# Kernel optimization log

Measured on AMD Instinct MI355X. Metric: run time of the kernel, lower is better.

## Reference

```python
import jax, jax.numpy as jnp
import numpy as np

B, S, D = 2, 2048, 2048
H, DK, DV, L = 16, 128, 128, 64


def setup_inputs() -> dict:
    key = jax.random.key(0)
    ks = jax.random.split(key, 16)
    sc = lambda fan_in: 1.0 / np.sqrt(fan_in)
    inp = {
        "queries": jax.random.normal(ks[0], (B, S, D), jnp.float32),
        "keys": jax.random.normal(ks[1], (B, S, D), jnp.float32),
        "values": jax.random.normal(ks[2], (B, S, D), jnp.float32),
        # weights stored [in, out]
        "Wq": jax.random.normal(ks[3], (D, DK * H), jnp.float32) * sc(D),
        "bq": jnp.zeros((DK * H,), jnp.float32),
        "Wlk": jax.random.normal(ks[4], (D, L * H), jnp.float32) * sc(D),
        "blk": jnp.zeros((L * H,), jnp.float32),
        "Wlv": jax.random.normal(ks[5], (D, L * H), jnp.float32) * sc(D),
        "blv": jnp.zeros((L * H,), jnp.float32),
        "Wkr": jax.random.normal(ks[6], (L, DK), jnp.float32) * sc(L),
        "bkr": jnp.zeros((DK,), jnp.float32),
        "Wvr": jax.random.normal(ks[7], (L, DV), jnp.float32) * sc(L),
        "bvr": jnp.zeros((DV,), jnp.float32),
        "Wo": jax.random.normal(ks[8], (DV * H, D), jnp.float32) * sc(DV * H),
        "bo": jnp.zeros((D,), jnp.float32),
    }
    return inp


def reference(queries, keys, values, Wq, bq, Wlk, blk, Wlv, blv, Wkr, bkr, Wvr, bvr, Wo, bo):
    b, sq, _ = queries.shape
    sk = keys.shape[1]
    # query projection -> [b, h, sq, dk]
    q = (queries @ Wq + bq).reshape(b, sq, H, DK).transpose(0, 2, 1, 3)
    # low-rank latent KV -> [b, sk, h, L]
    lat_k = (keys @ Wlk + blk).reshape(b, sk, H, L)
    lat_v = (values @ Wlv + blv).reshape(b, sk, H, L)
    # reconstruction -> [b, h, sk, dk/dv]
    k = (lat_k @ Wkr + bkr).transpose(0, 2, 1, 3)
    v = (lat_v @ Wvr + bvr).transpose(0, 2, 1, 3)
    scores = jnp.einsum("bhqd,bhkd->bhqk", q, k) / np.sqrt(DK).astype(np.float32)
    causal = jnp.triu(jnp.ones((sq, sk), dtype=bool), k=1)
    scores = jnp.where(causal, -jnp.inf, scores)
    attn = jax.nn.softmax(scores, axis=-1)
    out = jnp.einsum("bhqk,bhkd->bhqd", attn, v)
    out = out.transpose(0, 2, 1, 3).reshape(b, sq, H * DV)
    return out @ Wo + bo
```

## Files before the change

kernel.cpp:

```cpp
#include <hip/hip_runtime.h>
#include <hip/hip_bf16.h>

#define B_SZ    2
#define S_LEN   2048
#define D_MODEL 2048
#define N_HEADS 16
#define D_HEAD  128
#define L_RANK  64
#define M_ROWS  (B_SZ * S_LEN)
#define KD      2048
#define NT      (KD / 32)

typedef short          bf16x8 __attribute__((ext_vector_type(8)));
typedef float          f32x4  __attribute__((ext_vector_type(4)));
typedef float          f32x16 __attribute__((ext_vector_type(16)));
typedef unsigned short us4v   __attribute__((ext_vector_type(4)));
typedef unsigned short us8v   __attribute__((ext_vector_type(8)));
typedef unsigned int   u32x4  __attribute__((ext_vector_type(4)));

#define SCALE_Q 0.127517432f

static __device__ __forceinline__ unsigned short f2bf(float f) {
    unsigned int u = __float_as_uint(f);
    u += 0x7FFFu + ((u >> 16) & 1u);
    return (unsigned short)(u >> 16);
}

static __device__ __forceinline__ void gload16(const void* g, void* l) {
    __builtin_amdgcn_global_load_lds(
        (const __attribute__((address_space(1))) unsigned int*)g,
        (__attribute__((address_space(3))) unsigned int*)l, 16, 0, 0);
}

static __device__ __forceinline__ float exp2_hw(float x) {
    float r; asm("v_exp_f32 %0, %1" : "=v"(r) : "v"(x)); return r;
}
static __device__ __forceinline__ unsigned int cvtpk_bf16(float a, float b) {
    unsigned int r; asm("v_cvt_pk_bf16_f32 %0, %1, %2" : "=v"(r) : "v"(a), "v"(b)); return r;
}

__global__ __launch_bounds__(256) void prep_kernel(
    const float* __restrict__ q_in, const float* __restrict__ k_in,
    const float* __restrict__ v_in,
    const float* __restrict__ Wq, const float* __restrict__ Wlk,
    const float* __restrict__ Wlv, const float* __restrict__ Wo,
    const float* __restrict__ Wkr, const float* __restrict__ Wvr,
    unsigned short* __restrict__ q_o, unsigned short* __restrict__ k_o,
    unsigned short* __restrict__ v_o,
    unsigned short* __restrict__ WqT, unsigned short* __restrict__ WlkT,
    unsigned short* __restrict__ WlvT, unsigned short* __restrict__ WoT,
    unsigned short* __restrict__ WkrT, unsigned short* __restrict__ WvrT)
{
    __shared__ float tl[64][69];
    const int bid = blockIdx.x, tid = threadIdx.x;

    if (bid < 12288) {
        const int z = bid >> 12;
        const float* in = z == 0 ? q_in : (z == 1 ? k_in : v_in);
        unsigned short* out = z == 0 ? q_o : (z == 1 ? k_o : v_o);
        size_t i = ((size_t)(bid & 4095) * 256 + tid) * 8;
        float4 a = *(const float4*)&in[i];
        float4 b = *(const float4*)&in[i + 4];
        us8v o = { f2bf(a.x), f2bf(a.y), f2bf(a.z), f2bf(a.w),
                   f2bf(b.x), f2bf(b.y), f2bf(b.z), f2bf(b.w) };
        *(us8v*)&out[i] = o;
    } else if (bid < 16384) {
        const int t = bid - 12288;
        const int z = t >> 10;
        const int y = (t & 1023) >> 5, x = t & 31;
        const int Nz = (z == 1 || z == 2) ? 1024 : 2048;
        if (x * 64 >= Nz) return;
        const float* W = z == 0 ? Wq : (z == 1 ? Wlk : (z == 2 ? Wlv : Wo));
        unsigned short* WT = z == 0 ? WqT : (z == 1 ? WlkT : (z == 2 ? WlvT : WoT));
        const int k0 = y * 64, n0 = x * 64;
        #pragma unroll
        for (int c = 0; c < 4; ++c) {
            int idx = c * 256 + tid;
            int r = idx >> 4, c4 = (idx & 15) * 4;
            float4 v = *(const float4*)&W[(size_t)(k0 + r) * Nz + n0 + c4];
            tl[r][c4] = v.x; tl[r][c4 + 1] = v.y; tl[r][c4 + 2] = v.z; tl[r][c4 + 3] = v.w;
        }
        __syncthreads();
        #pragma unroll
        for (int c = 0; c < 2; ++c) {
            int idx = c * 256 + tid;
            int nr = idx >> 3, s = idx & 7;
            us8v o;
            #pragma unroll
            for (int j = 0; j < 8; ++j) o[j] = f2bf(tl[s * 8 + j][nr]);
            *(us8v*)&WT[(size_t)(n0 + nr) * KD + k0 + s * 8] = o;
        }
    } else {
        #pragma unroll 1
        for (int t2 = 0; t2 < 2; ++t2) {
            const float* W = t2 ? Wvr : Wkr;
            unsigned short* WT = t2 ? WvrT : WkrT;
            for (int i = 0; i < 32; ++i) {
                int e = i * 256 + tid;
                int d = e >> 6, l = e & 63;
                WT[d * 64 + l] = f2bf(W[l * 128 + d]);
            }
        }
    }
}

__global__ __launch_bounds__(256) void stage1_kernel(
    const unsigned short* __restrict__ Aq, const unsigned short* __restrict__ Ak,
    const unsigned short* __restrict__ Av,
    const unsigned short* __restrict__ WqT, const unsigned short* __restrict__ WlkT,
    const unsigned short* __restrict__ WlvT,
    const float* __restrict__ bq, const float* __restrict__ blk,
    const float* __restrict__ blv,
    unsigned short* __restrict__ q_bf, unsigned short* __restrict__ lat_k,
    unsigned short* __restrict__ lat_v)
{
    __shared__ unsigned short Al[2][128 * 32];
    __shared__ unsigned short Bl[2][128 * 32];

    const int flat = blockIdx.x;
    const int swz = (flat & 7) * 128 + (flat >> 3);
    int z, rem;
    if (swz < 512)      { z = 0; rem = swz; }
    else if (swz < 768) { z = 1; rem = swz - 512; }
    else                { z = 2; rem = swz - 768; }
    int row0, col0, Nz;
    if (z == 0) { row0 = (rem >> 4) * 128; col0 = (rem & 15) * 128; Nz = 2048; }
    else        { row0 = (rem >> 3) * 128; col0 = (rem & 7) * 128;  Nz = 1024; }

    const unsigned short* A    = z == 0 ? Aq  : (z == 1 ? Ak   : Av);
    const unsigned short* Bt   = z == 0 ? WqT : (z == 1 ? WlkT : WlvT);
    const float*          bias = z == 0 ? bq  : (z == 1 ? blk  : blv);
    unsigned short*       C    = z == 0 ? q_bf : (z == 1 ? lat_k : lat_v);

    const int tid = threadIdx.x;
    const int lane = tid & 63, wid = tid >> 6;
    const int lr = lane & 15, lg = lane >> 4;
    const int wr = wid >> 1, wc = wid & 1;

    const unsigned short* ag[2];
    const unsigned short* bg[2];
    unsigned short* alp[2][2];
    unsigned short* blp[2][2];
    #pragma unroll
    for (int c = 0; c < 2; ++c) {
        int idx = wid * 128 + c * 64 + lane;
        int row = idx >> 2, p = idx & 3;
        int sp = p ^ ((row >> 1) & 3);
        ag[c] = A  + (size_t)(row0 + row) * KD + sp * 8;
        bg[c] = Bt + (size_t)(col0 + row) * KD + sp * 8;
        alp[0][c] = Al[0] + idx * 8;  alp[1][c] = Al[1] + idx * 8;
        blp[0][c] = Bl[0] + idx * 8;  blp[1][c] = Bl[1] + idx * 8;
    }
    const int sx = (lr >> 1) & 3;
    const int abase = (wr * 64 + lr) * 32 + ((lg ^ sx) * 8);
    const int bbase = (wc * 64 + lr) * 32 + ((lg ^ sx) * 8);

    f32x4 acc[4][4];
    #pragma unroll
    for (int m = 0; m < 4; ++m)
        #pragma unroll
        for (int n = 0; n < 4; ++n) acc[m][n] = (f32x4){0.f, 0.f, 0.f, 0.f};

    #pragma unroll
    for (int c = 0; c < 2; ++c) { gload16(ag[c], alp[0][c]); gload16(bg[c], blp[0][c]); }
    __syncthreads();

    #pragma unroll 1
    for (int t = 0; t < NT; ++t) {
        const int cur = t & 1, nxt = cur ^ 1;
        if (t + 1 < NT) {
            #pragma unroll
            for (int c = 0; c < 2; ++c) {
                gload16(ag[c] + (size_t)(t + 1) * 32, alp[nxt][c]);
                gload16(bg[c] + (size_t)(t + 1) * 32, blp[nxt][c]);
            }
        }
        bf16x8 af[4], bfv[4];
        #pragma unroll
        for (int m = 0; m < 4; ++m) af[m]  = *(const bf16x8*)&Al[cur][abase + m * 512];
        #pragma unroll
        for (int n = 0; n < 4; ++n) bfv[n] = *(const bf16x8*)&Bl[cur][bbase + n * 512];
        __builtin_amdgcn_s_setprio(1);
        #pragma unroll
        for (int m = 0; m < 4; ++m)
            #pragma unroll
            for (int n = 0; n < 4; ++n)
                acc[m][n] = __builtin_amdgcn_mfma_f32_16x16x32_bf16(af[m], bfv[n], acc[m][n], 0, 0, 0);
        __builtin_amdgcn_s_setprio(0);
        __syncthreads();
    }

    float bv[4];
    #pragma unroll
    for (int n = 0; n < 4; ++n) bv[n] = bias[col0 + wc * 64 + n * 16 + lr];
    const float omul = (z == 0) ? SCALE_Q : 1.0f;

    #pragma unroll
    for (int m = 0; m < 4; ++m) {
        #pragma unroll
        for (int n = 0; n < 4; ++n) {
            const int col = col0 + wc * 64 + n * 16 + lr;
            const int rowb = row0 + wr * 64 + m * 16 + lg * 4;
            #pragma unroll
            for (int j = 0; j < 4; ++j)
                C[(size_t)(rowb + j) * Nz + col] = f2bf((acc[m][n][j] + bv[n]) * omul);
        }
    }
}

__global__ __launch_bounds__(256) void recon_kernel(
    const unsigned short* __restrict__ lat_k, const unsigned short* __restrict__ lat_v,
    const unsigned short* __restrict__ WkrT, const unsigned short* __restrict__ WvrT,
    const float* __restrict__ bkr, const float* __restrict__ bvr,
    unsigned short* __restrict__ k_bf, unsigned short* __restrict__ v_t)
{
    __shared__ unsigned short Alds[128 * 64];
    __shared__ unsigned short Blds[128 * 64];

    const int flat = blockIdx.x;
    const int swz = (flat & 7) * 128 + (flat >> 3);
    const int z = swz >> 9;
    const int rem = swz & 511;
    const int h = rem >> 5;
    const int r0 = (rem & 31) * 128;

    const unsigned short* lat = z ? lat_v : lat_k;
    const unsigned short* WT  = z ? WvrT : WkrT;
    const float* bias = z ? bvr : bkr;

    const int tid = threadIdx.x;
    const int lane = tid & 63, wid = tid >> 6;
    const int lr = lane & 15, lg = lane >> 4;
    const int wm = wid >> 1, wn = wid & 1;

    #pragma unroll
    for (int c = 0; c < 4; ++c) {
        int e = c * 256 + tid;
        int row = e >> 3, pc = e & 7;
        gload16(lat + (size_t)(r0 + row) * 1024 + h * 64 + ((pc ^ (row & 7)) * 8),
                Alds + e * 8);
    }
    #pragma unroll
    for (int c = 0; c < 4; ++c) {
        int e = c * 256 + tid;
        int d = e >> 3, pc = e & 7;
        gload16(WT + (size_t)d * 64 + ((pc ^ (d & 7)) * 8), Blds + e * 8);
    }
    __syncthreads();

    f32x4 acc[4][4];
    #pragma unroll
    for (int m = 0; m < 4; ++m)
        #pragma unroll
        for (int n = 0; n < 4; ++n) acc[m][n] = (f32x4){0.f, 0.f, 0.f, 0.f};

    #pragma unroll
    for (int ks = 0; ks < 2; ++ks) {
        bf16x8 af[4], bfv[4];
        #pragma unroll
        for (int m = 0; m < 4; ++m) {
            int row = wm * 64 + m * 16 + lr;
            af[m] = *(const bf16x8*)&Alds[row * 64 + (((ks * 4 + lg) ^ (row & 7)) * 8)];
        }
        #pragma unroll
        for (int n = 0; n < 4; ++n) {
            int row = wn * 64 + n * 16 + lr;
            bfv[n] = *(const bf16x8*)&Blds[row * 64 + (((ks * 4 + lg) ^ (row & 7)) * 8)];
        }
        #pragma unroll
        for (int m = 0; m < 4; ++m)
            #pragma unroll
            for (int n = 0; n < 4; ++n)
                acc[m][n] = __builtin_amdgcn_mfma_f32_16x16x32_bf16(af[m], bfv[n], acc[m][n], 0, 0, 0);
    }

    const int b = r0 >> 11;
    float bv[4];
    #pragma unroll
    for (int n = 0; n < 4; ++n) bv[n] = bias[wn * 64 + n * 16 + lr];

    #pragma unroll
    for (int m = 0; m < 4; ++m) {
        #pragma unroll
        for (int n = 0; n < 4; ++n) {
            const int d = wn * 64 + n * 16 + lr;
            const int rowb = r0 + wm * 64 + m * 16 + lg * 4;
            if (z == 0) {
                #pragma unroll
                for (int j = 0; j < 4; ++j)
                    k_bf[(size_t)(rowb + j) * D_MODEL + h * D_HEAD + d] =
                        f2bf(acc[m][n][j] + bv[n]);
            } else {
                us4v o = { f2bf(acc[m][n][0] + bv[n]), f2bf(acc[m][n][1] + bv[n]),
                           f2bf(acc[m][n][2] + bv[n]), f2bf(acc[m][n][3] + bv[n]) };
                *(us4v*)&v_t[((size_t)(b * 16 + h) * 128 + d) * 2048 + (rowb & 2047)] = o;
            }
        }
    }
}

__global__ __launch_bounds__(256) void out_gemm_kernel(
    const unsigned short* __restrict__ A,
    const unsigned short* __restrict__ Bt,
    const float* __restrict__ bias,
    float* __restrict__ C)
{
    __shared__ unsigned short Al[2][128 * 32];
    __shared__ unsigned short Bl[2][128 * 32];

    const int flat = blockIdx.x;
    const int swz = (flat & 7) * 64 + (flat >> 3);
    const int row0 = (swz >> 4) * 128, col0 = (swz & 15) * 128;

    const int tid = threadIdx.x;
    const int lane = tid & 63, wid = tid >> 6;
    const int lr = lane & 15, lg = lane >> 4;
    const int wr = wid >> 1, wc = wid & 1;

    const unsigned short* ag[2];
    const unsigned short* bg[2];
    unsigned short* alp[2][2];
    unsigned short* blp[2][2];
    #pragma unroll
    for (int c = 0; c < 2; ++c) {
        int idx = wid * 128 + c * 64 + lane;
        int row = idx >> 2, p = idx & 3;
        int sp = p ^ ((row >> 1) & 3);
        ag[c] = A  + (size_t)(row0 + row) * KD + sp * 8;
        bg[c] = Bt + (size_t)(col0 + row) * KD + sp * 8;
        alp[0][c] = Al[0] + idx * 8;  alp[1][c] = Al[1] + idx * 8;
        blp[0][c] = Bl[0] + idx * 8;  blp[1][c] = Bl[1] + idx * 8;
    }
    const int sx = (lr >> 1) & 3;
    const int abase = (wr * 64 + lr) * 32 + ((lg ^ sx) * 8);
    const int bbase = (wc * 64 + lr) * 32 + ((lg ^ sx) * 8);

    f32x4 acc[4][4];
    #pragma unroll
    for (int m = 0; m < 4; ++m)
        #pragma unroll
        for (int n = 0; n < 4; ++n) acc[m][n] = (f32x4){0.f, 0.f, 0.f, 0.f};

    #pragma unroll
    for (int c = 0; c < 2; ++c) { gload16(ag[c], alp[0][c]); gload16(bg[c], blp[0][c]); }
    __syncthreads();

    #pragma unroll 1
    for (int t = 0; t < NT; ++t) {
        const int cur = t & 1, nxt = cur ^ 1;
        if (t + 1 < NT) {
            #pragma unroll
            for (int c = 0; c < 2; ++c) {
                gload16(ag[c] + (size_t)(t + 1) * 32, alp[nxt][c]);
                gload16(bg[c] + (size_t)(t + 1) * 32, blp[nxt][c]);
            }
        }
        bf16x8 af[4], bfv[4];
        #pragma unroll
        for (int m = 0; m < 4; ++m) af[m]  = *(const bf16x8*)&Al[cur][abase + m * 512];
        #pragma unroll
        for (int n = 0; n < 4; ++n) bfv[n] = *(const bf16x8*)&Bl[cur][bbase + n * 512];
        __builtin_amdgcn_s_setprio(1);
        #pragma unroll
        for (int m = 0; m < 4; ++m)
            #pragma unroll
            for (int n = 0; n < 4; ++n)
                acc[m][n] = __builtin_amdgcn_mfma_f32_16x16x32_bf16(af[m], bfv[n], acc[m][n], 0, 0, 0);
        __builtin_amdgcn_s_setprio(0);
        __syncthreads();
    }

    float bv[4];
    #pragma unroll
    for (int n = 0; n < 4; ++n) bv[n] = bias[col0 + wc * 64 + n * 16 + lr];
    #pragma unroll
    for (int m = 0; m < 4; ++m)
        #pragma unroll
        for (int n = 0; n < 4; ++n) {
            const int col = col0 + wc * 64 + n * 16 + lr;
            const int rowb = row0 + wr * 64 + m * 16 + lg * 4;
            #pragma unroll
            for (int j = 0; j < 4; ++j)
                C[(size_t)(rowb + j) * D_MODEL + col] = acc[m][n][j] + bv[n];
        }
}

static __device__ __forceinline__ void flash_stage(
    const unsigned short* __restrict__ kgh,
    const unsigned short* __restrict__ vtb,
    unsigned short* Kl, unsigned short* Vl, int kv0, int tid)
{
    #pragma unroll
    for (int c = 0; c < 4; ++c) {
        int idx = c * 256 + tid;
        int r = idx >> 4, ch = idx & 15;
        gload16(kgh + (size_t)(kv0 + r) * D_MODEL + ((ch ^ (r & 7)) * 8), Kl + idx * 8);
    }
    #pragma unroll
    for (int c = 0; c < 4; ++c) {
        int idx = c * 256 + tid;
        int d = idx >> 3, ch = idx & 7;
        gload16(vtb + (size_t)d * S_LEN + kv0 + ((ch ^ (d & 7)) * 8), Vl + idx * 8);
    }
}

__global__ __launch_bounds__(256, 2) void flash_kernel(
    const unsigned short* __restrict__ Q,
    const unsigned short* __restrict__ Kg,
    const unsigned short* __restrict__ Vt,
    unsigned short* __restrict__ Og)
{
    __shared__ unsigned short Klds[2][64 * 128];
    __shared__ unsigned short Vlds[2][128 * 64];

    const int tid = threadIdx.x;
    const int lane = tid & 63, wid = tid >> 6;
    const int lc = lane & 31, hi = lane >> 5;

    const int blk = blockIdx.x;
    const int jj = blk >> 5;
    const int qt = (jj < 8) ? (15 - jj) : (jj - 8);
    const int bh = blk & 31;
    const int b = bh >> 4, h = bh & 15;
    const size_t base = (size_t)b * S_LEN * D_MODEL;
    const unsigned short* kgh = Kg + base + h * D_HEAD;
    const unsigned short* vtb = Vt + (size_t)bh * D_HEAD * S_LEN;

    const int q0w = qt * 128 + wid * 32;
    const int qcol = q0w + lc;

    bf16x8 qf[8];
    #pragma unroll
    for (int dc = 0; dc < 8; ++dc)
        qf[dc] = *(const bf16x8*)&Q[base + (size_t)qcol * D_MODEL + h * D_HEAD + dc * 16 + hi * 8];

    f32x16 o_acc[4];
    #pragma unroll
    for (int dt = 0; dt < 4; ++dt)
        #pragma unroll
        for (int r = 0; r < 16; ++r) o_acc[dt][r] = 0.f;
    float m_r = -3e38f, l_r = 0.f;

    const int kxor = lc & 7;
    const int nt = 2 * qt + 2;

    flash_stage(kgh, vtb, Klds[0], Vlds[0], 0, tid);

    #pragma unroll 1
    for (int t = 0; t < nt; ++t) {
        const int bb = t & 1;
        const int kv0 = t * 64;
        __syncthreads();
        if (t + 1 < nt)
            flash_stage(kgh, vtb, Klds[bb ^ 1], Vlds[bb ^ 1], (t + 1) * 64, tid);

        f32x16 s0a, s0b, s1a, s1b;
        #pragma unroll
        for (int r = 0; r < 16; ++r) { s0a[r] = 0.f; s0b[r] = 0.f; s1a[r] = 0.f; s1b[r] = 0.f; }
        __builtin_amdgcn_s_setprio(1);
        #pragma unroll
        for (int dc = 0; dc < 4; ++dc) {
            bf16x8 kf0 = *(const bf16x8*)&Klds[bb][lc * 128 + (((dc * 2 + hi) ^ kxor) * 8)];
            bf16x8 kf1 = *(const bf16x8*)&Klds[bb][(32 + lc) * 128 + (((dc * 2 + hi) ^ kxor) * 8)];
            s0a = __builtin_amdgcn_mfma_f32_32x32x16_bf16(kf0, qf[dc], s0a, 0, 0, 0);
            s1a = __builtin_amdgcn_mfma_f32_32x32x16_bf16(kf1, qf[dc], s1a, 0, 0, 0);
        }
        #pragma unroll
        for (int dc = 4; dc < 8; ++dc) {
            bf16x8 kf0 = *(const bf16x8*)&Klds[bb][lc * 128 + (((dc * 2 + hi) ^ kxor) * 8)];
            bf16x8 kf1 = *(const bf16x8*)&Klds[bb][(32 + lc) * 128 + (((dc * 2 + hi) ^ kxor) * 8)];
            s0b = __builtin_amdgcn_mfma_f32_32x32x16_bf16(kf0, qf[dc], s0b, 0, 0, 0);
            s1b = __builtin_amdgcn_mfma_f32_32x32x16_bf16(kf1, qf[dc], s1b, 0, 0, 0);
        }
        __builtin_amdgcn_s_setprio(0);
        f32x16 s0 = s0a + s0b;
        f32x16 s1 = s1a + s1b;

        if (t >= nt - 2) {
            #pragma unroll
            for (int r = 0; r < 16; ++r) {
                int krow = (r & 3) + 8 * (r >> 2) + 4 * hi;
                if (kv0 + krow > qcol)      s0[r] = -3e38f;
                if (kv0 + 32 + krow > qcol) s1[r] = -3e38f;
            }
        }

        float mt[8];
        #pragma unroll
        for (int i = 0; i < 8; ++i)
            mt[i] = fmaxf(fmaxf(s0[2 * i], s0[2 * i + 1]), fmaxf(s1[2 * i], s1[2 * i + 1]));
        float mA = fmaxf(fmaxf(mt[0], mt[1]), fmaxf(mt[2], mt[3]));
        float mB = fmaxf(fmaxf(mt[4], mt[5]), fmaxf(mt[6], mt[7]));
        float sm = fmaxf(mA, mB);
        sm = fmaxf(sm, __shfl_xor(sm, 32));

        if (__any(sm > m_r + 11.5f)) {
            float mnew = fmaxf(m_r, sm);
            float alpha = exp2_hw(m_r - mnew);
            l_r *= alpha;
            m_r = mnew;
            #pragma unroll
            for (int r = 0; r < 16; ++r) {
                float av = __shfl(alpha, (r & 3) + 8 * (r >> 2) + 4 * hi);
                #pragma unroll
                for (int dt = 0; dt < 4; ++dt) o_acc[dt][r] *= av;
            }
        }

        #pragma unroll
        for (int r = 0; r < 16; ++r) {
            s0[r] = exp2_hw(s0[r] - m_r);
            s1[r] = exp2_hw(s1[r] - m_r);
        }
        float st[8];
        #pragma unroll
        for (int i = 0; i < 8; ++i)
            st[i] = (s0[2 * i] + s0[2 * i + 1]) + (s1[2 * i] + s1[2 * i + 1]);
        l_r += ((st[0] + st[1]) + (st[2] + st[3])) + ((st[4] + st[5]) + (st[6] + st[7]));

        #pragma unroll
        for (int t32 = 0; t32 < 2; ++t32) {
            const f32x16& s = t32 ? s1 : s0;
            unsigned int c0[4], c1[4];
            #pragma unroll
            for (int g = 0; g < 4; ++g) {
                c0[g] = cvtpk_bf16(s[4 * g],     s[4 * g + 1]);
                c1[g] = cvtpk_bf16(s[4 * g + 2], s[4 * g + 3]);
            }
            #pragma unroll
            for (int kt = 0; kt < 2; ++kt) {
                unsigned int sel0 = hi ? c0[2 * kt] : c0[2 * kt + 1];
                unsigned int sel1 = hi ? c1[2 * kt] : c1[2 * kt + 1];
                unsigned int o0 = (unsigned int)__shfl_xor((int)sel0, 32);
                unsigned int o1 = (unsigned int)__shfl_xor((int)sel1, 32);
                u32x4 uu;
                uu.x = hi ? o0 : c0[2 * kt];
                uu.y = hi ? o1 : c1[2 * kt];
                uu.z = hi ? c0[2 * kt + 1] : o0;
                uu.w = hi ? c1[2 * kt + 1] : o1;
                bf16x8 pf = __builtin_bit_cast(bf16x8, uu);
                __builtin_amdgcn_s_setprio(1);
                #pragma unroll
                for (int dt = 0; dt < 4; ++dt) {
                    bf16x8 vf = *(const bf16x8*)
                        &Vlds[bb][(dt * 32 + lc) * 64 + (((t32 * 4 + kt * 2 + hi) ^ kxor) * 8)];
                    o_acc[dt] = __builtin_amdgcn_mfma_f32_32x32x16_bf16(pf, vf, o_acc[dt], 0, 0, 0);
                }
                __builtin_amdgcn_s_setprio(0);
            }
        }
    }

    float lt = l_r + __shfl_xor(l_r, 32);
    float inv = 1.0f / lt;
    #pragma unroll
    for (int r = 0; r < 16; ++r) {
        int qrow = (r & 3) + 8 * (r >> 2) + 4 * hi;
        float iv = __shfl(inv, qrow);
        #pragma unroll
        for (int dt = 0; dt < 4; ++dt)
            Og[base + (size_t)(q0w + qrow) * D_MODEL + h * D_HEAD + dt * 32 + lc] =
                f2bf(o_acc[dt][r] * iv);
    }
}

extern "C" void kernel_launch(void* const* d_in, const int* in_sizes, int n_in,
                              void* d_out, int out_size, void* d_ws, size_t ws_size,
                              hipStream_t stream)
{
    const float* queries = (const float*)d_in[0];
    const float* keys    = (const float*)d_in[1];
    const float* values  = (const float*)d_in[2];
    const float* Wq  = (const float*)d_in[3];
    const float* bq  = (const float*)d_in[4];
    const float* Wlk = (const float*)d_in[5];
    const float* blk = (const float*)d_in[6];
    const float* Wlv = (const float*)d_in[7];
    const float* blv = (const float*)d_in[8];
    const float* Wkr = (const float*)d_in[9];
    const float* bkr = (const float*)d_in[10];
    const float* Wvr = (const float*)d_in[11];
    const float* bvr = (const float*)d_in[12];
    const float* Wo  = (const float*)d_in[13];
    const float* bo  = (const float*)d_in[14];
    float* out = (float*)d_out;

    char* ws = (char*)d_ws;
    const size_t MB = 1024 * 1024;
    unsigned short* abf_q = (unsigned short*)(ws);
    unsigned short* abf_k = (unsigned short*)(ws + 16 * MB);
    unsigned short* abf_v = (unsigned short*)(ws + 32 * MB);
    unsigned short* q_bf  = (unsigned short*)(ws + 48 * MB);
    unsigned short* k_bf  = (unsigned short*)(ws + 64 * MB);
    unsigned short* v_t   = (unsigned short*)(ws + 80 * MB);
    unsigned short* lat_k = (unsigned short*)(ws + 96 * MB);
    unsigned short* lat_v = (unsigned short*)(ws + 104 * MB);
    unsigned short* WqT   = (unsigned short*)(ws + 112 * MB);
    unsigned short* WlkT  = (unsigned short*)(ws + 120 * MB);
    unsigned short* WlvT  = (unsigned short*)(ws + 124 * MB);
    unsigned short* WkrT  = (unsigned short*)(ws + 128 * MB);
    unsigned short* WvrT  = WkrT + 128 * 64;
    unsigned short* WoT   = (unsigned short*)(ws + 129 * MB);
    unsigned short* ao    = abf_q;

    prep_kernel<<<16385, 256, 0, stream>>>(
        queries, keys, values, Wq, Wlk, Wlv, Wo, Wkr, Wvr,
        abf_q, abf_k, abf_v, WqT, WlkT, WlvT, WoT, WkrT, WvrT);

    stage1_kernel<<<1024, 256, 0, stream>>>(
        abf_q, abf_k, abf_v, WqT, WlkT, WlvT, bq, blk, blv,
        q_bf, lat_k, lat_v);

    recon_kernel<<<1024, 256, 0, stream>>>(
        lat_k, lat_v, WkrT, WvrT, bkr, bvr, k_bf, v_t);

    flash_kernel<<<512, 256, 0, stream>>>(q_bf, k_bf, v_t, ao);

    out_gemm_kernel<<<512, 256, 0, stream>>>(ao, WoT, bo, out);
}
```

Before: 269.4 us.

## Rewrite projection GEMM as 256x256 tile, 8-wave, phased pipelined kernel

The fused Q/latent-K/latent-V projection GEMM moves from 128x128 tiles with 4 waves to 256x256 tiles with 8 waves, 512 threads and 256 blocks. K steps grow to 64 and are split into two 32-wide halves. Global-to-LDS loads are interleaved with MFMA phases using explicit vmcnt/lgkmcnt waits, raw barriers and inline ds_read_b128. The aim is more operand reuse per LDS byte and overlap of loads with MFMAs. The cost is more registers (a 32-tile accumulator per wave) and only 256 blocks, which may leave CUs underused.

```diff
diff --git a/kernel.cpp b/kernel.cpp
--- a/kernel.cpp
+++ b/kernel.cpp
@@ -10,6 +10,7 @@
 #define M_ROWS  (B_SZ * S_LEN)
 #define KD      2048
 #define NT      (KD / 32)
+#define NTK     (KD / 64)
 
 typedef short          bf16x8 __attribute__((ext_vector_type(8)));
 typedef float          f32x4  __attribute__((ext_vector_type(4)));
@@ -30,6 +31,14 @@
     __builtin_amdgcn_global_load_lds(
         (const __attribute__((address_space(1))) unsigned int*)g,
         (__attribute__((address_space(3))) unsigned int*)l, 16, 0, 0);
+}
+
+static __device__ __forceinline__ bf16x8 ds_read128(const unsigned short* p) {
+    bf16x8 r;
+    unsigned int a = (unsigned int)(size_t)
+        (const __attribute__((address_space(3))) unsigned short*)p;
+    asm volatile("ds_read_b128 %0, %1" : "=&v"(r) : "v"(a));
+    return r;
 }
 
 static __device__ __forceinline__ float exp2_hw(float x) {
@@ -104,7 +113,7 @@
     }
 }
 
-__global__ __launch_bounds__(256) void stage1_kernel(
+__global__ __launch_bounds__(512) void stage1_8p_kernel(
     const unsigned short* __restrict__ Aq, const unsigned short* __restrict__ Ak,
     const unsigned short* __restrict__ Av,
     const unsigned short* __restrict__ WqT, const unsigned short* __restrict__ WlkT,
@@ -114,18 +123,15 @@
     unsigned short* __restrict__ q_bf, unsigned short* __restrict__ lat_k,
     unsigned short* __restrict__ lat_v)
 {
-    __shared__ unsigned short Al[2][128 * 32];
-    __shared__ unsigned short Bl[2][128 * 32];
-
-    const int flat = blockIdx.x;
-    const int swz = (flat & 7) * 128 + (flat >> 3);
-    int z, rem;
-    if (swz < 512)      { z = 0; rem = swz; }
-    else if (swz < 768) { z = 1; rem = swz - 512; }
-    else                { z = 2; rem = swz - 768; }
-    int row0, col0, Nz;
-    if (z == 0) { row0 = (rem >> 4) * 128; col0 = (rem & 15) * 128; Nz = 2048; }
-    else        { row0 = (rem >> 3) * 128; col0 = (rem & 7) * 128;  Nz = 1024; }
+    __shared__ unsigned short Al[2][2][256 * 32];
+    __shared__ unsigned short Bl[2][2][256 * 32];
+
+    const int bid = blockIdx.x;
+    const int swz = (bid & 7) * 32 + (bid >> 3);
+    int z, rem, row0, col0, Nz;
+    if (swz < 128)      { z = 0; rem = swz;       row0 = (rem >> 3) * 256; col0 = (rem & 7) * 256; Nz = 2048; }
+    else if (swz < 192) { z = 1; rem = swz - 128; row0 = (rem >> 2) * 256; col0 = (rem & 3) * 256; Nz = 1024; }
+    else                { z = 2; rem = swz - 192; row0 = (rem >> 2) * 256; col0 = (rem & 3) * 256; Nz = 1024; }
 
     const unsigned short* A    = z == 0 ? Aq  : (z == 1 ? Ak   : Av);
     const unsigned short* Bt   = z == 0 ? WqT : (z == 1 ? WlkT : WlvT);
@@ -135,72 +141,130 @@
     const int tid = threadIdx.x;
     const int lane = tid & 63, wid = tid >> 6;
     const int lr = lane & 15, lg = lane >> 4;
-    const int wr = wid >> 1, wc = wid & 1;
-
-    const unsigned short* ag[2];
-    const unsigned short* bg[2];
-    unsigned short* alp[2][2];
-    unsigned short* blp[2][2];
-    #pragma unroll
-    for (int c = 0; c < 2; ++c) {
-        int idx = wid * 128 + c * 64 + lane;
-        int row = idx >> 2, p = idx & 3;
-        int sp = p ^ ((row >> 1) & 3);
-        ag[c] = A  + (size_t)(row0 + row) * KD + sp * 8;
-        bg[c] = Bt + (size_t)(col0 + row) * KD + sp * 8;
-        alp[0][c] = Al[0] + idx * 8;  alp[1][c] = Al[1] + idx * 8;
-        blp[0][c] = Bl[0] + idx * 8;  blp[1][c] = Bl[1] + idx * 8;
-    }
-    const int sx = (lr >> 1) & 3;
-    const int abase = (wr * 64 + lr) * 32 + ((lg ^ sx) * 8);
-    const int bbase = (wc * 64 + lr) * 32 + ((lg ^ sx) * 8);
-
-    f32x4 acc[4][4];
-    #pragma unroll
-    for (int m = 0; m < 4; ++m)
+    const int wm = wid >> 2, wn = wid & 3;
+
+    const int lin0 = tid, lin1 = 512 + tid;
+    const int rS0 = lin0 >> 2, rS1 = lin1 >> 2;
+    const int cS0 = (lin0 & 3) ^ ((rS0 >> 1) & 3);
+    const int cS1 = (lin1 & 3) ^ ((rS1 >> 1) & 3);
+    const unsigned short* aS0 = A  + (size_t)(row0 + rS0) * KD + cS0 * 8;
+    const unsigned short* aS1 = A  + (size_t)(row0 + rS1) * KD + cS1 * 8;
+    const unsigned short* bS0 = Bt + (size_t)(col0 + rS0) * KD + cS0 * 8;
+    const unsigned short* bS1 = Bt + (size_t)(col0 + rS1) * KD + cS1 * 8;
+    const int d0 = lin0 * 8, d1 = lin1 * 8;
+
+    int aoff[8], boff[4];
+    #pragma unroll
+    for (int m = 0; m < 8; ++m) {
+        int row = wm * 128 + m * 16 + lr;
+        aoff[m] = row * 32 + ((lg ^ ((row >> 1) & 3)) * 8);
+    }
+    #pragma unroll
+    for (int n = 0; n < 4; ++n) {
+        int row = wn * 64 + n * 16 + lr;
+        boff[n] = row * 32 + ((lg ^ ((row >> 1) & 3)) * 8);
+    }
+
+    f32x4 acc[8][4];
+    #pragma unroll
+    for (int m = 0; m < 8; ++m)
         #pragma unroll
         for (int n = 0; n < 4; ++n) acc[m][n] = (f32x4){0.f, 0.f, 0.f, 0.f};
 
-    #pragma unroll
-    for (int c = 0; c < 2; ++c) { gload16(ag[c], alp[0][c]); gload16(bg[c], blp[0][c]); }
-    __syncthreads();
+#define STAGE_A(buf, kh, kt) do { \
+        gload16(aS0 + (size_t)(kt) * 64 + (kh) * 32, &Al[buf][kh][d0]); \
+        gload16(aS1 + (size_t)(kt) * 64 + (kh) * 32, &Al[buf][kh][d1]); } while (0)
+#define STAGE_B(buf, kh, kt) do { \
+        gload16(bS0 + (size_t)(kt) * 64 + (kh) * 32, &Bl[buf][kh][d0]); \
+        gload16(bS1 + (size_t)(kt) * 64 + (kh) * 32, &Bl[buf][kh][d1]); } while (0)
+
+    STAGE_A(0, 0, 0); STAGE_B(0, 0, 0); STAGE_A(0, 1, 0); STAGE_B(0, 1, 0);
 
     #pragma unroll 1
-    for (int t = 0; t < NT; ++t) {
+    for (int t = 0; t < NTK; ++t) {
         const int cur = t & 1, nxt = cur ^ 1;
-        if (t + 1 < NT) {
-            #pragma unroll
-            for (int c = 0; c < 2; ++c) {
-                gload16(ag[c] + (size_t)(t + 1) * 32, alp[nxt][c]);
-                gload16(bg[c] + (size_t)(t + 1) * 32, blp[nxt][c]);
-            }
-        }
-        bf16x8 af[4], bfv[4];
-        #pragma unroll
-        for (int m = 0; m < 4; ++m) af[m]  = *(const bf16x8*)&Al[cur][abase + m * 512];
-        #pragma unroll
-        for (int n = 0; n < 4; ++n) bfv[n] = *(const bf16x8*)&Bl[cur][bbase + n * 512];
+        const bool more = (t + 1 < NTK);
+
+        asm volatile("s_waitcnt vmcnt(4)" ::: "memory");
+        __builtin_amdgcn_s_barrier();
+        asm volatile("" ::: "memory");
+
+        bf16x8 af[8], bf0, bf1;
+        if (more) STAGE_A(nxt, 0, t + 1);
+        #pragma unroll
+        for (int m = 0; m < 8; ++m) af[m] = ds_read128(&Al[cur][0][aoff[m]]);
+        bf0 = ds_read128(&Bl[cur][0][boff[0]]);
+        bf1 = ds_read128(&Bl[cur][0][boff[1]]);
+        asm volatile("s_waitcnt lgkmcnt(0)" ::: "memory");
+        __builtin_amdgcn_sched_barrier(0);
         __builtin_amdgcn_s_setprio(1);
         #pragma unroll
-        for (int m = 0; m < 4; ++m)
-            #pragma unroll
-            for (int n = 0; n < 4; ++n)
-                acc[m][n] = __builtin_amdgcn_mfma_f32_16x16x32_bf16(af[m], bfv[n], acc[m][n], 0, 0, 0);
+        for (int m = 0; m < 8; ++m) {
+            acc[m][0] = __builtin_amdgcn_mfma_f32_16x16x32_bf16(af[m], bf0, acc[m][0], 0, 0, 0);
+            acc[m][1] = __builtin_amdgcn_mfma_f32_16x16x32_bf16(af[m], bf1, acc[m][1], 0, 0, 0);
+        }
         __builtin_amdgcn_s_setprio(0);
-        __syncthreads();
-    }
+
+        if (more) STAGE_B(nxt, 0, t + 1);
+        bf0 = ds_read128(&Bl[cur][0][boff[2]]);
+        bf1 = ds_read128(&Bl[cur][0][boff[3]]);
+        asm volatile("s_waitcnt lgkmcnt(0)" ::: "memory");
+        __builtin_amdgcn_sched_barrier(0);
+        __builtin_amdgcn_s_setprio(1);
+        #pragma unroll
+        for (int m = 0; m < 8; ++m) {
+            acc[m][2] = __builtin_amdgcn_mfma_f32_16x16x32_bf16(af[m], bf0, acc[m][2], 0, 0, 0);
+            acc[m][3] = __builtin_amdgcn_mfma_f32_16x16x32_bf16(af[m], bf1, acc[m][3], 0, 0, 0);
+        }
+        __builtin_amdgcn_s_setprio(0);
+
+        if (more) asm volatile("s_waitcnt vmcnt(4)" ::: "memory");
+        else      asm volatile("s_waitcnt vmcnt(0)" ::: "memory");
+        __builtin_amdgcn_s_barrier();
+        asm volatile("" ::: "memory");
+
+        if (more) STAGE_A(nxt, 1, t + 1);
+        #pragma unroll
+        for (int m = 0; m < 8; ++m) af[m] = ds_read128(&Al[cur][1][aoff[m]]);
+        bf0 = ds_read128(&Bl[cur][1][boff[0]]);
+        bf1 = ds_read128(&Bl[cur][1][boff[1]]);
+        asm volatile("s_waitcnt lgkmcnt(0)" ::: "memory");
+        __builtin_amdgcn_sched_barrier(0);
+        __builtin_amdgcn_s_setprio(1);
+        #pragma unroll
+        for (int m = 0; m < 8; ++m) {
+            acc[m][0] = __builtin_amdgcn_mfma_f32_16x16x32_bf16(af[m], bf0, acc[m][0], 0, 0, 0);
+            acc[m][1] = __builtin_amdgcn_mfma_f32_16x16x32_bf16(af[m], bf1, acc[m][1], 0, 0, 0);
+        }
+        __builtin_amdgcn_s_setprio(0);
+
+        if (more) STAGE_B(nxt, 1, t + 1);
+        bf0 = ds_read128(&Bl[cur][1][boff[2]]);
+        bf1 = ds_read128(&Bl[cur][1][boff[3]]);
+        asm volatile("s_waitcnt lgkmcnt(0)" ::: "memory");
+        __builtin_amdgcn_sched_barrier(0);
+        __builtin_amdgcn_s_setprio(1);
+        #pragma unroll
+        for (int m = 0; m < 8; ++m) {
+            acc[m][2] = __builtin_amdgcn_mfma_f32_16x16x32_bf16(af[m], bf0, acc[m][2], 0, 0, 0);
+            acc[m][3] = __builtin_amdgcn_mfma_f32_16x16x32_bf16(af[m], bf1, acc[m][3], 0, 0, 0);
+        }
+        __builtin_amdgcn_s_setprio(0);
+    }
+#undef STAGE_A
+#undef STAGE_B
 
     float bv[4];
     #pragma unroll
-    for (int n = 0; n < 4; ++n) bv[n] = bias[col0 + wc * 64 + n * 16 + lr];
+    for (int n = 0; n < 4; ++n) bv[n] = bias[col0 + wn * 64 + n * 16 + lr];
     const float omul = (z == 0) ? SCALE_Q : 1.0f;
 
     #pragma unroll
-    for (int m = 0; m < 4; ++m) {
+    for (int m = 0; m < 8; ++m) {
         #pragma unroll
         for (int n = 0; n < 4; ++n) {
-            const int col = col0 + wc * 64 + n * 16 + lr;
-            const int rowb = row0 + wr * 64 + m * 16 + lg * 4;
+            const int col = col0 + wn * 64 + n * 16 + lr;
+            const int rowb = row0 + wm * 128 + m * 16 + lg * 4;
             #pragma unroll
             for (int j = 0; j < 4; ++j)
                 C[(size_t)(rowb + j) * Nz + col] = f2bf((acc[m][n][j] + bv[n]) * omul);
@@ -607,7 +671,7 @@
         queries, keys, values, Wq, Wlk, Wlv, Wo, Wkr, Wvr,
         abf_q, abf_k, abf_v, WqT, WlkT, WlvT, WoT, WkrT, WvrT);
 
-    stage1_kernel<<<1024, 256, 0, stream>>>(
+    stage1_8p_kernel<<<256, 512, 0, stream>>>(
         abf_q, abf_k, abf_v, WqT, WlkT, WlvT, bq, blk, blv,
         q_bf, lat_k, lat_v);
 
```

After: 242.2 us. -10.1%, faster.
